# Kernel optimization log

Hardware: AMD Instinct MI355X
Metric: run time of the kernel (lower is better)

The kernel has to match this reference:

```python
import jax, jax.numpy as jnp
import numpy as np

GROUPS = 8
EPS = 1e-5


def group_norm(x, gamma, beta):
    # x: [B,H,W,C]; normalize per group over (H, W, C/g)
    B, H, W, C = x.shape
    g = GROUPS
    xg = x.reshape(B, H, W, g, C // g)
    mean = jnp.mean(xg, axis=(1, 2, 4), keepdims=True)
    var = jnp.var(xg, axis=(1, 2, 4), keepdims=True)
    xg = (xg - mean) / jnp.sqrt(var + EPS)
    return gamma * xg.reshape(B, H, W, C) + beta


def setup_inputs() -> dict:
    key = jax.random.key(0)
    ks = jax.random.split(key, 6)
    B, H, W, C = 8, 64, 64, 128
    s = 1.0 / np.sqrt(C)
    return {
        "x": jax.random.normal(ks[0], (B, H, W, C), jnp.float32),
        "gamma": jnp.ones((C,), jnp.float32),
        "beta": jnp.zeros((C,), jnp.float32),
        "wq": jax.random.normal(ks[1], (C, C), jnp.float32) * s,
        "bq": jnp.zeros((C,), jnp.float32),
        "wk": jax.random.normal(ks[2], (C, C), jnp.float32) * s,
        "bk": jnp.zeros((C,), jnp.float32),
        "wv": jax.random.normal(ks[3], (C, C), jnp.float32) * s,
        "bv": jnp.zeros((C,), jnp.float32),
        "wp": jax.random.normal(ks[4], (C, C), jnp.float32) * s,
        "bp": jnp.zeros((C,), jnp.float32),
    }


def reference(x, gamma, beta, wq, bq, wk, bk, wv, bv, wp, bp):
    B, H, W, C = x.shape
    scale = jnp.asarray(C, jnp.float32) ** -0.5
    xn = group_norm(x, gamma, beta)  # note: residual uses normalized input (as in source)
    N = H * W
    xf = xn.reshape(B, N, C)
    q = xf @ wq + bq
    k = xf @ wk + bk
    v = xf @ wv + bv
    attn = jnp.einsum('bnc,bmc->bnm', q, k) * scale  # [B, N, N]
    attn = jax.nn.softmax(attn, axis=-1)
    out = jnp.einsum('bnm,bmc->bnc', attn, v)
    out = out @ wp + bp
    return (xf + out).reshape(B, H, W, C)
```

## Files before the change

### kernel.cpp

```cpp
#include <hip/hip_runtime.h>
#include <hip/hip_bf16.h>

#define B_ 8
#define N_ 4096
#define C_ 128
#define EPSV 1e-5f
#define SPLIT 3
#define KVB 64

using bf8   = __attribute__((ext_vector_type(8))) short;
using u16x8 = __attribute__((ext_vector_type(8))) ushort;
using f32x4 = __attribute__((ext_vector_type(4))) float;

__device__ __forceinline__ ushort f2b(float f) {
  __hip_bfloat16 h = __float2bfloat16(f);
  return *reinterpret_cast<ushort*>(&h);
}
__device__ __forceinline__ float b2f(ushort u) {
  union { float f; unsigned x; } t; t.x = ((unsigned)u) << 16; return t.f;
}

__device__ __forceinline__ void gll16(const void* g, void* l) {
  __builtin_amdgcn_global_load_lds((const __attribute__((address_space(1))) void*)g,
                                   (__attribute__((address_space(3))) void*)l,
                                   16, 0, 0);
}

__global__ __launch_bounds__(256) void gnw(const float* __restrict__ x,
                                           const float* __restrict__ wq,
                                           const float* __restrict__ wk,
                                           const float* __restrict__ wv,
                                           const float* __restrict__ wp,
                                           float2* __restrict__ part,
                                           ushort* __restrict__ wt) {
  if (blockIdx.y >= 64) {
    const int widx = blockIdx.y - 64;
    const float* w = (widx == 0) ? wq : (widx == 1) ? wk : (widx == 2) ? wv : wp;
    ushort* o = wt + widx * 16384;
    const int r  = blockIdx.x * 16 + (threadIdx.x >> 4);
    const int c0 = (threadIdx.x & 15) << 3;
    const float4 v0 = *reinterpret_cast<const float4*>(w + (size_t)r * C_ + c0);
    const float4 v1 = *reinterpret_cast<const float4*>(w + (size_t)r * C_ + c0 + 4);
    const float vv[8] = {v0.x, v0.y, v0.z, v0.w, v1.x, v1.y, v1.z, v1.w};
    #pragma unroll
    for (int j = 0; j < 8; ++j) {
      const int n = c0 + j;
      const int el = (r & 7) | ((((r >> 3)) ^ (n & 7)) << 3);
      o[(size_t)n * C_ + el] = f2b(vv[j]);
    }
    return;
  }
  const int bg = blockIdx.y;
  const int b = bg >> 3, g = bg & 7;
  const int chunk = blockIdx.x;
  const float* xp = x + (size_t)b * N_ * C_ + g * 16;
  float s = 0.f, s2 = 0.f;
  const int base4 = chunk * 2048;
  for (int i = threadIdx.x; i < 2048; i += 256) {
    const int idx = base4 + i;
    const int n = idx >> 2, c4 = (idx & 3) << 2;
    const float4 v = *reinterpret_cast<const float4*>(xp + (size_t)n * C_ + c4);
    s  += v.x + v.y + v.z + v.w;
    s2 += v.x*v.x + v.y*v.y + v.z*v.z + v.w*v.w;
  }
  #pragma unroll
  for (int off = 32; off; off >>= 1) { s += __shfl_down(s, off); s2 += __shfl_down(s2, off); }
  __shared__ float red[8];
  const int wid = threadIdx.x >> 6;
  if ((threadIdx.x & 63) == 0) { red[wid] = s; red[4 + wid] = s2; }
  __syncthreads();
  if (threadIdx.x == 0)
    part[bg * 8 + chunk] = make_float2(red[0]+red[1]+red[2]+red[3],
                                       red[4]+red[5]+red[6]+red[7]);
}

__device__ __forceinline__ void block_mrs(const float2* part, int b, int tid,
                                          float2* sp, float* mrs) {
  if (tid < 64) sp[tid] = part[b * 64 + tid];
  __syncthreads();
  if (tid < 8) {
    float s = 0.f, s2 = 0.f;
    #pragma unroll
    for (int c = 0; c < 8; ++c) { s += sp[tid*8+c].x; s2 += sp[tid*8+c].y; }
    const float inv = 1.f / 65536.f;
    const float m = s * inv;
    const float var = s2 * inv - m * m;
    mrs[tid*2]   = m;
    mrs[tid*2+1] = rsqrtf(var + EPSV);
  }
  __syncthreads();
}

__global__ __launch_bounds__(256) void qkv_fused(const float* __restrict__ x,
                                                 const float2* __restrict__ part,
                                                 const float* __restrict__ gamma,
                                                 const float* __restrict__ beta,
                                                 const ushort* __restrict__ wt,
                                                 const float* __restrict__ bq,
                                                 const float* __restrict__ bk,
                                                 const float* __restrict__ bv,
                                                 ushort* __restrict__ qb, ushort* __restrict__ kb,
                                                 ushort* __restrict__ vtb) {
  __shared__ ushort A[64][128];
  __shared__ ushort Bt[128][128];
  __shared__ float2 sp[64];
  __shared__ float mrs[16];
  const int m0 = blockIdx.x * 64;
  const int tid = threadIdx.x;
  const int wid = tid >> 6, lane = tid & 63;
  block_mrs(part, m0 >> 12, tid, sp, mrs);
  for (int i = tid; i < 1024; i += 256) {
    const int row = i >> 4, c = (i & 15) << 3;
    const int grow = m0 + row;
    const float mm = mrs[(c >> 4) * 2], rr = mrs[(c >> 4) * 2 + 1];
    const float4 v0 = *reinterpret_cast<const float4*>(&x[(size_t)grow * C_ + c]);
    const float4 v1 = *reinterpret_cast<const float4*>(&x[(size_t)grow * C_ + c + 4]);
    const float vv[8] = {v0.x, v0.y, v0.z, v0.w, v1.x, v1.y, v1.z, v1.w};
    u16x8 u;
    #pragma unroll
    for (int j = 0; j < 8; ++j)
      u[j] = f2b((vv[j] - mm) * rr * gamma[c+j] + beta[c+j]);
    const int el = ((c >> 3) ^ (row & 7)) << 3;
    *reinterpret_cast<u16x8*>(&A[row][el]) = u;
  }
  const int wm = wid >> 1, wn = wid & 1;
  const int lr = lane & 15, lk = lane >> 4;
  const float qscale = 0.12751749f;

  #pragma unroll 1
  for (int j = 0; j < 3; ++j) {
    const ushort* wtj = wt + j * 16384;
    const float* bias = (j == 0) ? bq : (j == 1) ? bk : bv;
    __syncthreads();
    {
      ushort* bt0 = &Bt[0][0];
      #pragma unroll
      for (int c8 = 0; c8 < 8; ++c8) {
        const int ch = wid * 8 + c8;
        gll16(wtj + ch * 512 + lane * 8, bt0 + ch * 512);
      }
    }
    __syncthreads();
    f32x4 acc[2][4] = {};
    #pragma unroll
    for (int ks = 0; ks < 4; ++ks) {
      const int g0 = ks * 4 + lk;
      bf8 af[2], bfv[4];
      #pragma unroll
      for (int mi = 0; mi < 2; ++mi) {
        const int row = wm * 32 + mi * 16 + lr;
        af[mi] = *reinterpret_cast<const bf8*>(&A[row][(g0 ^ (row & 7)) << 3]);
      }
      #pragma unroll
      for (int ni = 0; ni < 4; ++ni) {
        const int n = wn * 64 + ni * 16 + lr;
        bfv[ni] = *reinterpret_cast<const bf8*>(&Bt[n][(g0 ^ (n & 7)) << 3]);
      }
      #pragma unroll
      for (int mi = 0; mi < 2; ++mi)
        #pragma unroll
        for (int ni = 0; ni < 4; ++ni)
          acc[mi][ni] = __builtin_amdgcn_mfma_f32_16x16x32_bf16(af[mi], bfv[ni], acc[mi][ni], 0, 0, 0);
    }
    if (j < 2) {
      ushort* out = (j == 0) ? qb : kb;
      const float sc = (j == 0) ? qscale : 1.0f;
      #pragma unroll
      for (int mi = 0; mi < 2; ++mi)
        #pragma unroll
        for (int ni = 0; ni < 4; ++ni)
          #pragma unroll
          for (int r = 0; r < 4; ++r) {
            const int row = m0 + wm * 32 + mi * 16 + lk * 4 + r;
            const int col = wn * 64 + ni * 16 + lr;
            out[(size_t)row * C_ + col] = f2b((acc[mi][ni][r] + bias[col]) * sc);
          }
    } else {
      #pragma unroll
      for (int mi = 0; mi < 2; ++mi)
        #pragma unroll
        for (int ni = 0; ni < 4; ++ni) {
          const int rowb = m0 + wm * 32 + mi * 16 + lk * 4;
          const int col  = wn * 64 + ni * 16 + lr;
          const int bb = rowb >> 12, nn = rowb & 4095;
          const int o  = nn & 63;
          const int op = (o & 0x23) | ((o & 0x0C) << 1) | ((o & 0x10) >> 2);
          const int nnp = (nn & ~63) | op;
          const float bv2 = bias[col];
          ushort4 u;
          u.x = f2b(acc[mi][ni][0] + bv2);
          u.y = f2b(acc[mi][ni][1] + bv2);
          u.z = f2b(acc[mi][ni][2] + bv2);
          u.w = f2b(acc[mi][ni][3] + bv2);
          *reinterpret_cast<ushort4*>(&vtb[((size_t)bb * C_ + col) * N_ + nnp]) = u;
        }
    }
  }
}

__global__ __launch_bounds__(256, 3) void attn_fwd(const ushort* __restrict__ q,
                                                   const ushort* __restrict__ k,
                                                   const ushort* __restrict__ vt,
                                                   ushort* __restrict__ Op,
                                                   float* __restrict__ lsum) {
  extern __shared__ ushort smem[];
  const int bid = blockIdx.x;
  const int b   = bid & 7;
  const int qi  = (bid >> 3) & 31;
  const int z   = bid >> 8;
  const int q0  = qi * 128;
  const int tid = threadIdx.x;
  const int w = tid >> 6, lane = tid & 63;
  const int lr = lane & 15, lk = lane >> 4;
  const ushort* qb = q  + (size_t)b * N_ * C_;
  const ushort* kb = k  + (size_t)b * N_ * C_;
  const ushort* vb = vt + (size_t)b * C_ * N_;

  bf8 qf[2][4];
  #pragma unroll
  for (int h = 0; h < 2; ++h) {
    const int qrow = q0 + w * 32 + h * 16 + lr;
    #pragma unroll
    for (int ks = 0; ks < 4; ++ks)
      qf[h][ks] = *reinterpret_cast<const bf8*>(&qb[(size_t)qrow * C_ + ks * 32 + lk * 8]);
  }

  bf8 onesf;
  #pragma unroll
  for (int j = 0; j < 8; ++j) onesf[j] = (short)0x3F80;

  f32x4 oacc[2][8] = {};
  f32x4 accl[2] = {};

  const int krow_in = lane >> 4;
  const int kslot   = lane & 15;
  const int vrow_in = lane >> 3;
  const int vslot   = lane & 7;

  const int t0 = (z * 64) / SPLIT;
  const int t1 = ((z + 1) * 64) / SPLIT;

  auto STAGE_K = [&](int sel, int kt) {
    const int kv0 = kt * KVB;
    ushort* Kd = smem + sel * 8192;
    #pragma unroll
    for (int j = 0; j < 4; ++j) {
      const int m = w * 4 + j;
      const int krow = m * 4 + krow_in;
      gll16(kb + (size_t)(kv0 + krow) * C_ + ((kslot ^ (krow & 7)) << 3),
            Kd + m * 512);
    }
  };
  auto STAGE_V = [&](int kt) {
    const int kv0 = kt * KVB;
    ushort* Vd = smem + 16384;
    #pragma unroll
    for (int j = 0; j < 4; ++j) {
      const int m = w * 4 + j;
      const int vrow = m * 8 + vrow_in;
      gll16(vb + (size_t)vrow * N_ + kv0 + ((vslot ^ (vrow & 7)) << 3),
            Vd + m * 512);
    }
  };

  STAGE_K(0, t0);
  __builtin_amdgcn_s_setprio(1);
  for (int kt = t0; kt < t1; ++kt) {
    const int cur = (kt - t0) & 1;
    __syncthreads();
    STAGE_V(kt);
    if (kt + 1 < t1) STAGE_K(cur ^ 1, kt + 1);

    const ushort* Kc = smem + cur * 8192;
    const ushort* Vc = smem + 16384;

    f32x4 s[2][4] = {};
    bf8 kf[2][4];
    #pragma unroll
    for (int ni = 0; ni < 4; ++ni) {
      const int n = ni * 16 + lr;
      kf[0][ni] = *reinterpret_cast<const bf8*>(&Kc[n * 128 + ((lk ^ (n & 7)) << 3)]);
    }
    #pragma unroll
    for (int ks = 0; ks < 4; ++ks) {
      const int cb = ks & 1;
      if (ks < 3) {
        const int g1 = (ks + 1) * 4 + lk;
        #pragma unroll
        for (int ni = 0; ni < 4; ++ni) {
          const int n = ni * 16 + lr;
          kf[cb ^ 1][ni] = *reinterpret_cast<const bf8*>(&Kc[n * 128 + ((g1 ^ (n & 7)) << 3)]);
        }
      }
      #pragma unroll
      for (int h = 0; h < 2; ++h)
        #pragma unroll
        for (int ni = 0; ni < 4; ++ni)
          s[h][ni] = __builtin_amdgcn_mfma_f32_16x16x32_bf16(kf[cb][ni], qf[h][ks], s[h][ni], 0, 0, 0);
    }

    bf8 pa[2][2];
    #pragma unroll
    for (int kss = 0; kss < 2; ++kss)
      #pragma unroll
      for (int h = 0; h < 2; ++h) {
        bf8 t;
        #pragma unroll
        for (int hi = 0; hi < 2; ++hi) {
          const f32x4 sv = s[h][kss * 2 + hi];
          #pragma unroll
          for (int r = 0; r < 4; ++r)
            t[hi * 4 + r] = (short)f2b(__builtin_amdgcn_exp2f(sv[r]));
        }
        pa[kss][h] = t;
      }
    #pragma unroll
    for (int kss = 0; kss < 2; ++kss)
      #pragma unroll
      for (int h = 0; h < 2; ++h)
        accl[h] = __builtin_amdgcn_mfma_f32_16x16x32_bf16(pa[kss][h], onesf, accl[h], 0, 0, 0);

    __syncthreads();

    bf8 vf[8];
    #pragma unroll
    for (int ni = 0; ni < 8; ++ni) {
      const int d = ni * 16 + lr;
      vf[ni] = *reinterpret_cast<const bf8*>(&Vc[d * 64 + ((lk ^ (d & 7)) << 3)]);
    }
    #pragma unroll
    for (int kss = 0; kss < 2; ++kss) {
      #pragma unroll
      for (int h = 0; h < 2; ++h)
        #pragma unroll
        for (int ni = 0; ni < 8; ++ni)
          oacc[h][ni] = __builtin_amdgcn_mfma_f32_16x16x32_bf16(pa[kss][h], vf[ni], oacc[h][ni], 0, 0, 0);
      if (kss == 0) {
        #pragma unroll
        for (int ni = 0; ni < 8; ++ni) {
          const int d = ni * 16 + lr;
          vf[ni] = *reinterpret_cast<const bf8*>(&Vc[d * 64 + (((4 + lk) ^ (d & 7)) << 3)]);
        }
      }
    }
  }
  __builtin_amdgcn_s_setprio(0);

  const size_t zb = (size_t)(z * B_ + b);
  if (lr == 0) {
    #pragma unroll
    for (int h = 0; h < 2; ++h)
      #pragma unroll
      for (int r = 0; r < 4; ++r)
        lsum[zb * N_ + q0 + w * 32 + h * 16 + lk * 4 + r] = accl[h][r];
  }
  ushort* ob = Op + zb * N_ * C_;
  #pragma unroll
  for (int h = 0; h < 2; ++h)
    #pragma unroll
    for (int ni = 0; ni < 8; ++ni)
      #pragma unroll
      for (int r = 0; r < 4; ++r) {
        const int row = q0 + w * 32 + h * 16 + lk * 4 + r;
        ob[(size_t)row * C_ + ni * 16 + lr] = f2b(oacc[h][ni][r]);
      }
}

__global__ __launch_bounds__(256) void proj_res(const ushort* __restrict__ Op,
                                                const float* __restrict__ lsum,
                                                const ushort* __restrict__ wtp,
                                                const float* __restrict__ bias,
                                                const float* __restrict__ x,
                                                const float2* __restrict__ part,
                                                const float* __restrict__ gamma,
                                                const float* __restrict__ beta,
                                                float* __restrict__ outp) {
  __shared__ ushort A[64][128];
  __shared__ ushort Bt[128][128];
  __shared__ float2 sp[64];
  __shared__ float mrs[16];
  const int m0 = blockIdx.x * 64;
  const int tid = threadIdx.x;
  const int wid = tid >> 6, lane = tid & 63;
  const size_t BN = (size_t)B_ * N_;
  block_mrs(part, m0 >> 12, tid, sp, mrs);
  {
    ushort* bt0 = &Bt[0][0];
    #pragma unroll
    for (int c8 = 0; c8 < 8; ++c8) {
      const int ch = wid * 8 + c8;
      gll16(wtp + ch * 512 + lane * 8, bt0 + ch * 512);
    }
  }
  for (int i = tid; i < 1024; i += 256) {
    const int row = i >> 4, c = (i & 15) << 3;
    const size_t grow = m0 + row;
    float l = 0.f;
    #pragma unroll
    for (int zz = 0; zz < SPLIT; ++zz) l += lsum[zz * BN + grow];
    const float inv = 1.f / l;
    float acc8[8] = {};
    #pragma unroll
    for (int zz = 0; zz < SPLIT; ++zz) {
      const u16x8 a = *reinterpret_cast<const u16x8*>(&Op[(zz * BN + grow) * C_ + c]);
      #pragma unroll
      for (int j = 0; j < 8; ++j) acc8[j] += b2f(a[j]);
    }
    u16x8 u;
    #pragma unroll
    for (int j = 0; j < 8; ++j) u[j] = f2b(acc8[j] * inv);
    const int el = ((c >> 3) ^ (row & 7)) << 3;
    *reinterpret_cast<u16x8*>(&A[row][el]) = u;
  }
  __syncthreads();
  const int wm = wid >> 1, wn = wid & 1;
  const int lr = lane & 15, lk = lane >> 4;
  f32x4 acc[2][4] = {};
  #pragma unroll
  for (int ks = 0; ks < 4; ++ks) {
    const int g0 = ks * 4 + lk;
    bf8 af[2], bfv[4];
    #pragma unroll
    for (int mi = 0; mi < 2; ++mi) {
      const int row = wm * 32 + mi * 16 + lr;
      af[mi] = *reinterpret_cast<const bf8*>(&A[row][(g0 ^ (row & 7)) << 3]);
    }
    #pragma unroll
    for (int ni = 0; ni < 4; ++ni) {
      const int n = wn * 64 + ni * 16 + lr;
      bfv[ni] = *reinterpret_cast<const bf8*>(&Bt[n][(g0 ^ (n & 7)) << 3]);
    }
    #pragma unroll
    for (int mi = 0; mi < 2; ++mi)
      #pragma unroll
      for (int ni = 0; ni < 4; ++ni)
        acc[mi][ni] = __builtin_amdgcn_mfma_f32_16x16x32_bf16(af[mi], bfv[ni], acc[mi][ni], 0, 0, 0);
  }
  #pragma unroll
  for (int mi = 0; mi < 2; ++mi)
    #pragma unroll
    for (int ni = 0; ni < 4; ++ni) {
      const int col = wn * 64 + ni * 16 + lr;
      const float gmm = gamma[col], bta = beta[col], bia = bias[col];
      const float mm = mrs[(col >> 4) * 2], rr = mrs[(col >> 4) * 2 + 1];
      #pragma unroll
      for (int r = 0; r < 4; ++r) {
        const int row = m0 + wm * 32 + mi * 16 + lk * 4 + r;
        const float xn = (x[(size_t)row * C_ + col] - mm) * rr * gmm + bta;
        outp[(size_t)row * C_ + col] = xn + acc[mi][ni][r] + bia;
      }
    }
}

extern "C" void kernel_launch(void* const* d_in, const int* in_sizes, int n_in,
                              void* d_out, int out_size, void* d_ws, size_t ws_size,
                              hipStream_t stream) {
  const float* x     = (const float*)d_in[0];
  const float* gamma = (const float*)d_in[1];
  const float* beta  = (const float*)d_in[2];
  const float* wq    = (const float*)d_in[3];
  const float* bq    = (const float*)d_in[4];
  const float* wk    = (const float*)d_in[5];
  const float* bk    = (const float*)d_in[6];
  const float* wv    = (const float*)d_in[7];
  const float* bv    = (const float*)d_in[8];
  const float* wp    = (const float*)d_in[9];
  const float* bp    = (const float*)d_in[10];
  float* outp = (float*)d_out;

  char* ws = (char*)d_ws;
  const size_t MB8 = (size_t)B_ * N_ * C_ * 2;
  float2* part = (float2*)(ws + 512);
  ushort* qb   = (ushort*)(ws + 8192);
  ushort* kb   = (ushort*)(ws + 8192 + MB8);
  ushort* vtb  = (ushort*)(ws + 8192 + 2*MB8);
  ushort* Op   = (ushort*)(ws + 8192 + 3*MB8);
  float*  lsum = (float*)(ws + 8192 + (3 + SPLIT)*MB8);
  ushort* wt   = (ushort*)(ws + 8192 + (3 + SPLIT)*MB8 + (size_t)SPLIT*B_*N_*4);

  gnw<<<dim3(8, 68), 256, 0, stream>>>(x, wq, wk, wv, wp, part, wt);
  qkv_fused<<<512, 256, 0, stream>>>(x, part, gamma, beta, wt,
                                     bq, bk, bv, qb, kb, vtb);
  (void)hipFuncSetAttribute((const void*)attn_fwd,
                            hipFuncAttributeMaxDynamicSharedMemorySize, 49152);
  attn_fwd<<<dim3(32 * B_ * SPLIT), 256, 49152, stream>>>(qb, kb, vtb, Op, lsum);
  proj_res<<<512, 256, 0, stream>>>(Op, lsum, wt + 3 * 16384, bp, x, part, gamma, beta, outp);
}
```

Measured before the change: 112.2 us.

## Software-pipeline attention loop with double-buffered K/V and two-tile QK/PV overlap

Restructures the attention main loop to process two KV tiles per iteration. The QK^T of the next tile is interleaved with the softmax and PV of the current tile, and both K and V are double-buffered in LDS, which raises LDS to 64KB. The KV split drops from 3 to 2 and the occupancy hint goes from 3 to 2 blocks, so there is less partial-output traffic but fewer resident waves and fewer blocks. The s accumulators for two tiles increase register pressure.

```diff
diff --git a/kernel.cpp b/kernel.cpp
--- a/kernel.cpp
+++ b/kernel.cpp
@@ -5,7 +5,7 @@
 #define N_ 4096
 #define C_ 128
 #define EPSV 1e-5f
-#define SPLIT 3
+#define SPLIT 2
 #define KVB 64
 
 using bf8   = __attribute__((ext_vector_type(8))) short;
@@ -198,7 +198,7 @@
   }
 }
 
-__global__ __launch_bounds__(256, 3) void attn_fwd(const ushort* __restrict__ q,
+__global__ __launch_bounds__(256, 2) void attn_fwd(const ushort* __restrict__ q,
                                                    const ushort* __restrict__ k,
                                                    const ushort* __restrict__ vt,
                                                    ushort* __restrict__ Op,
@@ -237,8 +237,8 @@
   const int vrow_in = lane >> 3;
   const int vslot   = lane & 7;
 
-  const int t0 = (z * 64) / SPLIT;
-  const int t1 = ((z + 1) * 64) / SPLIT;
+  const int t0 = z * 32;
+  const int t1 = t0 + 32;
 
   auto STAGE_K = [&](int sel, int kt) {
     const int kv0 = kt * KVB;
@@ -251,9 +251,9 @@
             Kd + m * 512);
     }
   };
-  auto STAGE_V = [&](int kt) {
+  auto STAGE_V = [&](int sel, int kt) {
     const int kv0 = kt * KVB;
-    ushort* Vd = smem + 16384;
+    ushort* Vd = smem + 16384 + sel * 8192;
     #pragma unroll
     for (int j = 0; j < 4; ++j) {
       const int m = w * 4 + j;
@@ -263,42 +263,30 @@
     }
   };
 
-  STAGE_K(0, t0);
-  __builtin_amdgcn_s_setprio(1);
-  for (int kt = t0; kt < t1; ++kt) {
-    const int cur = (kt - t0) & 1;
-    __syncthreads();
-    STAGE_V(kt);
-    if (kt + 1 < t1) STAGE_K(cur ^ 1, kt + 1);
-
-    const ushort* Kc = smem + cur * 8192;
-    const ushort* Vc = smem + 16384;
-
-    f32x4 s[2][4] = {};
-    bf8 kf[2][4];
-    #pragma unroll
-    for (int ni = 0; ni < 4; ++ni) {
-      const int n = ni * 16 + lr;
-      kf[0][ni] = *reinterpret_cast<const bf8*>(&Kc[n * 128 + ((lk ^ (n & 7)) << 3)]);
-    }
+  auto QKT = [&](const ushort* Kc, f32x4 (&s)[2][4]) {
+    #pragma unroll
+    for (int h = 0; h < 2; ++h)
+      #pragma unroll
+      for (int ni = 0; ni < 4; ++ni)
+        s[h][ni] = (f32x4){0.f, 0.f, 0.f, 0.f};
     #pragma unroll
     for (int ks = 0; ks < 4; ++ks) {
-      const int cb = ks & 1;
-      if (ks < 3) {
-        const int g1 = (ks + 1) * 4 + lk;
-        #pragma unroll
-        for (int ni = 0; ni < 4; ++ni) {
-          const int n = ni * 16 + lr;
-          kf[cb ^ 1][ni] = *reinterpret_cast<const bf8*>(&Kc[n * 128 + ((g1 ^ (n & 7)) << 3)]);
-        }
+      const int g0 = ks * 4 + lk;
+      bf8 kf[4];
+      #pragma unroll
+      for (int ni = 0; ni < 4; ++ni) {
+        const int n = ni * 16 + lr;
+        kf[ni] = *reinterpret_cast<const bf8*>(&Kc[n * 128 + ((g0 ^ (n & 7)) << 3)]);
       }
       #pragma unroll
       for (int h = 0; h < 2; ++h)
         #pragma unroll
         for (int ni = 0; ni < 4; ++ni)
-          s[h][ni] = __builtin_amdgcn_mfma_f32_16x16x32_bf16(kf[cb][ni], qf[h][ks], s[h][ni], 0, 0, 0);
-    }
-
+          s[h][ni] = __builtin_amdgcn_mfma_f32_16x16x32_bf16(kf[ni], qf[h][ks], s[h][ni], 0, 0, 0);
+    }
+  };
+
+  auto SOFTPV = [&](f32x4 (&s)[2][4], const ushort* Vc) {
     bf8 pa[2][2];
     #pragma unroll
     for (int kss = 0; kss < 2; ++kss)
@@ -319,9 +307,6 @@
       #pragma unroll
       for (int h = 0; h < 2; ++h)
         accl[h] = __builtin_amdgcn_mfma_f32_16x16x32_bf16(pa[kss][h], onesf, accl[h], 0, 0, 0);
-
-    __syncthreads();
-
     bf8 vf[8];
     #pragma unroll
     for (int ni = 0; ni < 8; ++ni) {
@@ -343,6 +328,28 @@
         }
       }
     }
+  };
+
+  STAGE_K(0, t0);
+  STAGE_V(0, t0);
+  STAGE_K(1, t0 + 1);
+  __syncthreads();
+  f32x4 sA[2][4], sB[2][4];
+  QKT(smem, sA);
+
+  __builtin_amdgcn_s_setprio(1);
+  #pragma unroll 1
+  for (int t = t0; t < t1; t += 2) {
+    __syncthreads();
+    if (t + 2 < t1) STAGE_K(0, t + 2);
+    STAGE_V(1, t + 1);
+    QKT(smem + 8192, sB);
+    SOFTPV(sA, smem + 16384);
+    __syncthreads();
+    if (t + 3 < t1) STAGE_K(1, t + 3);
+    if (t + 2 < t1) STAGE_V(0, t + 2);
+    if (t + 2 < t1) QKT(smem, sA);
+    SOFTPV(sB, smem + 24576);
   }
   __builtin_amdgcn_s_setprio(0);
 
@@ -482,7 +489,7 @@
   qkv_fused<<<512, 256, 0, stream>>>(x, part, gamma, beta, wt,
                                      bq, bk, bv, qb, kb, vtb);
   (void)hipFuncSetAttribute((const void*)attn_fwd,
-                            hipFuncAttributeMaxDynamicSharedMemorySize, 49152);
-  attn_fwd<<<dim3(32 * B_ * SPLIT), 256, 49152, stream>>>(qb, kb, vtb, Op, lsum);
+                            hipFuncAttributeMaxDynamicSharedMemorySize, 65536);
+  attn_fwd<<<dim3(32 * B_ * SPLIT), 256, 65536, stream>>>(qb, kb, vtb, Op, lsum);
   proj_res<<<512, 256, 0, stream>>>(Op, lsum, wt + 3 * 16384, bp, x, part, gamma, beta, outp);
 }
```

Result: faster. 104.0 us (-7.3%).

## Single-buffer K and double-buffer V to restructure attention load pipeline

Applied to the files above, without the earlier changes.

Switches the shared-memory staging plan from double-buffered K with single-buffered V to single-buffered K with double-buffered V. The next tile's K and V loads are now issued right after the QK^T MFMAs finish reading K, so they overlap with the softmax and PV work. The kf register double-buffering is also removed and the loop is kept rolled. This moves the barriers around and may expose K load latency at the start of each iteration, and dropping the kf prefetch may stall the MFMAs on LDS reads.

```diff
diff --git a/kernel.cpp b/kernel.cpp
--- a/kernel.cpp
+++ b/kernel.cpp
@@ -240,20 +240,19 @@
   const int t0 = (z * 64) / SPLIT;
   const int t1 = ((z + 1) * 64) / SPLIT;
 
-  auto STAGE_K = [&](int sel, int kt) {
+  auto STAGE_K = [&](int kt) {
     const int kv0 = kt * KVB;
-    ushort* Kd = smem + sel * 8192;
     #pragma unroll
     for (int j = 0; j < 4; ++j) {
       const int m = w * 4 + j;
       const int krow = m * 4 + krow_in;
       gll16(kb + (size_t)(kv0 + krow) * C_ + ((kslot ^ (krow & 7)) << 3),
-            Kd + m * 512);
+            smem + m * 512);
     }
   };
-  auto STAGE_V = [&](int kt) {
+  auto STAGE_V = [&](int sel, int kt) {
     const int kv0 = kt * KVB;
-    ushort* Vd = smem + 16384;
+    ushort* Vd = smem + 8192 + sel * 8192;
     #pragma unroll
     for (int j = 0; j < 4; ++j) {
       const int m = w * 4 + j;
@@ -263,41 +262,33 @@
     }
   };
 
-  STAGE_K(0, t0);
+  STAGE_K(t0);
+  STAGE_V(0, t0);
+  __syncthreads();
   __builtin_amdgcn_s_setprio(1);
+  #pragma unroll 1
   for (int kt = t0; kt < t1; ++kt) {
     const int cur = (kt - t0) & 1;
+
+    f32x4 s[2][4] = {};
+    #pragma unroll
+    for (int ks = 0; ks < 4; ++ks) {
+      const int g0 = ks * 4 + lk;
+      bf8 kf[4];
+      #pragma unroll
+      for (int ni = 0; ni < 4; ++ni) {
+        const int n = ni * 16 + lr;
+        kf[ni] = *reinterpret_cast<const bf8*>(&smem[n * 128 + ((g0 ^ (n & 7)) << 3)]);
+      }
+      #pragma unroll
+      for (int h = 0; h < 2; ++h)
+        #pragma unroll
+        for (int ni = 0; ni < 4; ++ni)
+          s[h][ni] = __builtin_amdgcn_mfma_f32_16x16x32_bf16(kf[ni], qf[h][ks], s[h][ni], 0, 0, 0);
+    }
+
     __syncthreads();
-    STAGE_V(kt);
-    if (kt + 1 < t1) STAGE_K(cur ^ 1, kt + 1);
-
-    const ushort* Kc = smem + cur * 8192;
-    const ushort* Vc = smem + 16384;
-
-    f32x4 s[2][4] = {};
-    bf8 kf[2][4];
-    #pragma unroll
-    for (int ni = 0; ni < 4; ++ni) {
-      const int n = ni * 16 + lr;
-      kf[0][ni] = *reinterpret_cast<const bf8*>(&Kc[n * 128 + ((lk ^ (n & 7)) << 3)]);
-    }
-    #pragma unroll
-    for (int ks = 0; ks < 4; ++ks) {
-      const int cb = ks & 1;
-      if (ks < 3) {
-        const int g1 = (ks + 1) * 4 + lk;
-        #pragma unroll
-        for (int ni = 0; ni < 4; ++ni) {
-          const int n = ni * 16 + lr;
-          kf[cb ^ 1][ni] = *reinterpret_cast<const bf8*>(&Kc[n * 128 + ((g1 ^ (n & 7)) << 3)]);
-        }
-      }
-      #pragma unroll
-      for (int h = 0; h < 2; ++h)
-        #pragma unroll
-        for (int ni = 0; ni < 4; ++ni)
-          s[h][ni] = __builtin_amdgcn_mfma_f32_16x16x32_bf16(kf[cb][ni], qf[h][ks], s[h][ni], 0, 0, 0);
-    }
+    if (kt + 1 < t1) { STAGE_K(kt + 1); STAGE_V(cur ^ 1, kt + 1); }
 
     bf8 pa[2][2];
     #pragma unroll
@@ -320,8 +311,7 @@
       for (int h = 0; h < 2; ++h)
         accl[h] = __builtin_amdgcn_mfma_f32_16x16x32_bf16(pa[kss][h], onesf, accl[h], 0, 0, 0);
 
-    __syncthreads();
-
+    const ushort* Vc = smem + 8192 + cur * 8192;
     bf8 vf[8];
     #pragma unroll
     for (int ni = 0; ni < 8; ++ni) {
@@ -343,6 +333,8 @@
         }
       }
     }
+
+    __syncthreads();
   }
   __builtin_amdgcn_s_setprio(0);
 
```

Result: slower. 138.8 us (+23.7%).
